# Kernel optimization log

Hardware: AMD Instinct MI355X
Metric: run time of the kernel (lower is better)

The kernel has to match this reference:

```python
import jax, jax.numpy as jnp
import numpy as np

# Dimensions: B graphs, N padded nodes/graph, E edges/graph, D feature dim,
# H attention heads (concat=False -> head average), L stacked GAT layers.
B, N, E, D, H, L = 64, 1024, 16384, 300, 5, 2
NEG_SLOPE = 0.2   # PyG GATConv default negative_slope
LN_EPS = 1e-5


def setup_inputs() -> dict:
    key = jax.random.key(0)
    ks = jax.random.split(key, 6)
    t2 = jax.random.normal(ks[0], (B, N, D), dtype=jnp.float32)
    edge_index = jax.random.randint(ks[1], (B, 2, E), 0, N, dtype=jnp.int32)
    gnn_mask = jnp.zeros((B, N), dtype=bool)  # True = padded node
    # Per-layer GATConv parameters (heads=5, concat=False -> out dim D)
    W = jax.random.normal(ks[2], (L, D, H * D), dtype=jnp.float32) * 0.05
    att_src = jax.random.normal(ks[3], (L, H, D), dtype=jnp.float32) * 0.05
    att_dst = jax.random.normal(ks[4], (L, H, D), dtype=jnp.float32) * 0.05
    bias = jnp.zeros((L, D), dtype=jnp.float32)
    # Shared LayerNorm (single nn.LayerNorm reused after every layer)
    ln_gamma = jnp.ones((D,), dtype=jnp.float32)
    ln_beta = jnp.zeros((D,), dtype=jnp.float32)
    return {"t2": t2, "edge_index": edge_index, "gnn_mask": gnn_mask,
            "W": W, "att_src": att_src, "att_dst": att_dst, "bias": bias,
            "ln_gamma": ln_gamma, "ln_beta": ln_beta}


def _layernorm(x, g, b):
    mu = jnp.mean(x, axis=-1, keepdims=True)
    var = jnp.mean(jnp.square(x - mu), axis=-1, keepdims=True)
    return (x - mu) * jax.lax.rsqrt(var + LN_EPS) * g + b


def _gat_conv(x, src, dst, mask, Wl, a_src, a_dst, bl):
    """Single-graph GATConv: x[N,D], src/dst[E], mask[N] (True=padded)."""
    n = x.shape[0]
    h = (x @ Wl).reshape(n, H, D)                       # [N,H,D] projected per head
    a_s = jnp.einsum('nhd,hd->nh', h, a_src)            # [N,H]
    a_d = jnp.einsum('nhd,hd->nh', h, a_dst)            # [N,H]
    e = jax.nn.leaky_relu(a_s[src] + a_d[dst], NEG_SLOPE)  # [E,H] edge scores
    # drop messages originating from padded nodes
    e = jnp.where(mask[src][:, None], -1e9, e)
    # scatter-softmax over incoming edges of each destination node
    m = jax.ops.segment_max(e, dst, num_segments=n)     # [N,H]
    ex = jnp.exp(e - m[dst])
    den = jax.ops.segment_sum(ex, dst, num_segments=n)  # [N,H]
    alpha = ex / (den[dst] + 1e-16)                     # [E,H]
    # scatter-add aggregation of head-weighted messages
    out = jax.ops.segment_sum(alpha[:, :, None] * h[src], dst, num_segments=n)
    return out.mean(axis=1) + bl                        # concat=False: head mean, [N,D]


def reference(t2, edge_index, gnn_mask, W, att_src, att_dst, bias, ln_gamma, ln_beta):
    x = t2
    for l in range(L):
        conv = lambda xg, ei, mg: _gat_conv(xg, ei[0], ei[1], mg,
                                            W[l], att_src[l], att_dst[l], bias[l])
        x = jax.vmap(conv)(x, edge_index, gnn_mask)     # batch over graphs
        x = _layernorm(jax.nn.gelu(x), ln_gamma, ln_beta)  # GELU then shared LayerNorm
    return x
```

## Files before the change

### kernel.cpp

```cpp
#include <hip/hip_runtime.h>
#include <cstdint>
#include <cstddef>

typedef unsigned short u16;
typedef short short8 __attribute__((ext_vector_type(8)));
typedef __bf16 bf16x8 __attribute__((ext_vector_type(8)));
typedef float f32x4 __attribute__((ext_vector_type(4)));

#define BB 64
#define NNODE 1024
#define EDGES 16384
#define DIM 300
#define HEADS 5
#define LAYERS 2
#define K_PAD 320
#define N_PAD 1536
#define BM 128
#define BK 32

__device__ __forceinline__ u16 f32_to_bf16(float f) {
    union { float f; uint32_t u; } v; v.f = f;
    uint32_t u = v.u;
    uint32_t r = u + 0x7fffu + ((u >> 16) & 1u);
    return (u16)(r >> 16);
}
__device__ __forceinline__ float bf16_to_f32(u16 h) {
    union { uint32_t u; float f; } v; v.u = ((uint32_t)h) << 16;
    return v.f;
}

__global__ __launch_bounds__(256) void csr_build(const int* __restrict__ ei,
                                                 int* __restrict__ offs,
                                                 int* __restrict__ csr_src) {
    int b = blockIdx.x;
    const int* src = ei + (size_t)b * 2 * EDGES;
    const int* dst = src + EDGES;
    __shared__ int cnt[NNODE];
    __shared__ int grp[256];
    int t = threadIdx.x;
    for (int i = t; i < NNODE; i += 256) cnt[i] = 0;
    __syncthreads();
    for (int e = t; e < EDGES; e += 256) atomicAdd(&cnt[dst[e]], 1);
    __syncthreads();
    int c0 = cnt[4 * t + 0], c1 = cnt[4 * t + 1], c2 = cnt[4 * t + 2], c3 = cnt[4 * t + 3];
    grp[t] = c0 + c1 + c2 + c3;
    __syncthreads();
    for (int off = 1; off < 256; off <<= 1) {
        int v = (t >= off) ? grp[t - off] : 0;
        __syncthreads();
        grp[t] += v;
        __syncthreads();
    }
    int base = (t == 0) ? 0 : grp[t - 1];
    int o0 = base, o1 = o0 + c0, o2 = o1 + c1, o3 = o2 + c2;
    cnt[4 * t + 0] = o0; cnt[4 * t + 1] = o1; cnt[4 * t + 2] = o2; cnt[4 * t + 3] = o3;
    int* ob = offs + b * (NNODE + 1);
    ob[4 * t + 0] = o0; ob[4 * t + 1] = o1; ob[4 * t + 2] = o2; ob[4 * t + 3] = o3;
    if (t == 0) ob[NNODE] = EDGES;
    __syncthreads();
    for (int e = t; e < EDGES; e += 256) {
        int d = dst[e];
        int pos = atomicAdd(&cnt[d], 1);
        csr_src[(size_t)b * EDGES + pos] = src[e];
    }
}

__global__ __launch_bounds__(256) void split_w_all(const float* __restrict__ W,
                                                   u16* __restrict__ hi, u16* __restrict__ lo) {
    int i = blockIdx.x * 256 + threadIdx.x;
    int k = i % K_PAD;
    int rem = i / K_PAD;
    int n = rem % N_PAD;
    int l = rem / N_PAD;
    float v = (k < DIM && n < HEADS * DIM)
                  ? W[((size_t)l * DIM + k) * (HEADS * DIM) + n]
                  : 0.f;
    u16 h = f32_to_bf16(v);
    hi[i] = h;
    lo[i] = f32_to_bf16(v - bf16_to_f32(h));
}

__global__ __launch_bounds__(256) void pad_x(const float* __restrict__ X,
                                             float* __restrict__ Xp) {
    size_t i = (size_t)blockIdx.x * 256 + threadIdx.x;
    int k = (int)(i % K_PAD);
    size_t row = i / K_PAD;
    Xp[i] = (k < DIM) ? X[row * DIM + k] : 0.f;
}

__device__ __forceinline__ f32x4 mfma16(short8 a, short8 b, f32x4 c) {
    return __builtin_amdgcn_mfma_f32_16x16x32_bf16(
        __builtin_bit_cast(bf16x8, a), __builtin_bit_cast(bf16x8, b), c, 0, 0, 0);
}

__global__ __launch_bounds__(256) void gemm_split(const float* __restrict__ Xp,
                                                  const u16* __restrict__ Bhi,
                                                  const u16* __restrict__ Blo,
                                                  u16* __restrict__ Hout) {
    __shared__ __align__(16) short lds[4][BM][BK];
    int t = threadIdx.x;
    int m0 = blockIdx.x * BM, n0 = blockIdx.y * BM;
    int lane = t & 63, w = t >> 6, wr = w >> 1, wc = w & 1;
    int lrow = lane & 15, kg = lane >> 4;

    const u16* gWh = Bhi + (size_t)n0 * K_PAD;
    const u16* gWl = Blo + (size_t)n0 * K_PAD;

    f32x4 acc[4][4] = {};

    for (int k0 = 0; k0 < K_PAD; k0 += BK) {
        __syncthreads();
#pragma unroll
        for (int i = 0; i < 2; i++) {
            int chunk = t + (i << 8);
            int row = chunk >> 2, g = chunk & 3;
            const float* src = &Xp[(size_t)(m0 + row) * K_PAD + k0 + g * 8];
            f32x4 v0 = *(const f32x4*)src;
            f32x4 v1 = *(const f32x4*)(src + 4);
            short8 h8, l8;
#pragma unroll
            for (int j = 0; j < 8; j++) {
                float f = (j < 4) ? v0[j] : v1[j - 4];
                u16 h = f32_to_bf16(f);
                h8[j] = (short)h;
                l8[j] = (short)f32_to_bf16(f - bf16_to_f32(h));
            }
            int gsw = (g ^ ((row >> 1) & 3)) * 8;
            *(short8*)&lds[0][row][gsw] = h8;
            *(short8*)&lds[1][row][gsw] = l8;
        }
#pragma unroll
        for (int i = 0; i < 4; i++) {
            int chunk = t + ((i & 1) << 8);
            int row = chunk >> 2, g = chunk & 3;
            int gsw = (g ^ ((row >> 1) & 3)) * 8;
            const u16* gs = (i < 2) ? gWh : gWl;
            short* ls = (i < 2) ? &lds[2][row][gsw] : &lds[3][row][gsw];
            *(short8*)ls = *(const short8*)&gs[(size_t)row * K_PAD + k0 + g * 8];
        }
        __syncthreads();

        short8 ah[4], al[4], bh[4], bl[4];
#pragma unroll
        for (int f = 0; f < 4; f++) {
            int ra = wr * 64 + f * 16 + lrow;
            int sa = (kg ^ ((ra >> 1) & 3)) * 8;
            ah[f] = *(const short8*)&lds[0][ra][sa];
            al[f] = *(const short8*)&lds[1][ra][sa];
            int rb = wc * 64 + f * 16 + lrow;
            int sb = (kg ^ ((rb >> 1) & 3)) * 8;
            bh[f] = *(const short8*)&lds[2][rb][sb];
            bl[f] = *(const short8*)&lds[3][rb][sb];
        }
#pragma unroll
        for (int fm = 0; fm < 4; fm++)
#pragma unroll
            for (int fn = 0; fn < 4; fn++) {
                acc[fm][fn] = mfma16(ah[fm], bh[fn], acc[fm][fn]);
                acc[fm][fn] = mfma16(ah[fm], bl[fn], acc[fm][fn]);
                acc[fm][fn] = mfma16(al[fm], bh[fn], acc[fm][fn]);
            }
    }

#pragma unroll
    for (int fm = 0; fm < 4; fm++)
#pragma unroll
        for (int fn = 0; fn < 4; fn++)
#pragma unroll
            for (int i = 0; i < 4; i++) {
                int row = m0 + wr * 64 + fm * 16 + (lane >> 4) * 4 + i;
                int col = n0 + wc * 64 + fn * 16 + (lane & 15);
                Hout[(size_t)row * N_PAD + col] = f32_to_bf16(acc[fm][fn][i]);
            }
}

__global__ __launch_bounds__(256) void head_dots(const u16* __restrict__ Hb,
                                                 const float* __restrict__ att_s,
                                                 const float* __restrict__ att_d,
                                                 float* __restrict__ a_s,
                                                 float* __restrict__ a_d) {
    int node = blockIdx.x * 4 + (threadIdx.x >> 6);
    int lane = threadIdx.x & 63;
    const u16* row = Hb + (size_t)node * N_PAD;
#pragma unroll
    for (int hd = 0; hd < HEADS; hd++) {
        float ss = 0.f, sd = 0.f;
        for (int c = hd * DIM + lane; c < (hd + 1) * DIM; c += 64) {
            float hv = bf16_to_f32(row[c]);
            ss += hv * att_s[c];
            sd += hv * att_d[c];
        }
#pragma unroll
        for (int o = 32; o > 0; o >>= 1) {
            ss += __shfl_down(ss, o);
            sd += __shfl_down(sd, o);
        }
        if (lane == 0) {
            a_s[(size_t)node * HEADS + hd] = ss;
            a_d[(size_t)node * HEADS + hd] = sd;
        }
    }
}

__global__ __launch_bounds__(320) void agg_kernel(const u16* __restrict__ Hb,
                                                  const float* __restrict__ a_s,
                                                  const float* __restrict__ a_d_arr,
                                                  const int* __restrict__ offs,
                                                  const int* __restrict__ csr_src,
                                                  const unsigned char* __restrict__ mask,
                                                  const float* __restrict__ bias_l,
                                                  const float* __restrict__ gamma,
                                                  const float* __restrict__ beta,
                                                  int graph0,
                                                  float* __restrict__ out,
                                                  int ldo, int do_pad) {
    int nb = blockIdx.x;
    int xcd = nb & 7;
    int j = nb >> 3;
    int b = xcd + 8 * (j >> 10);
    int n = j & 1023;
    int node = b * NNODE + n;
    int gb = graph0 + b;
    int t = threadIdx.x;
    int h = t % 5, et = t / 5;

    __shared__ float red[320];
    __shared__ float mh[5], dh[5];
    __shared__ float alpha[64][5];
    __shared__ int srcs[64];
    __shared__ float stat[2];

    int off0 = offs[gb * (NNODE + 1) + n];
    int off1 = offs[gb * (NNODE + 1) + n + 1];
    int deg = off1 - off0;
    const int* slist = csr_src + (size_t)gb * EDGES + off0;
    float adh = a_d_arr[(size_t)node * HEADS + h];

    float mt = -1e30f;
    for (int e = et; e < deg; e += 64) {
        int s = slist[e];
        float sc = a_s[(size_t)(b * NNODE + s) * HEADS + h] + adh;
        sc = (sc >= 0.f) ? sc : 0.2f * sc;
        if (mask[gb * NNODE + s]) sc = -1e9f;
        mt = fmaxf(mt, sc);
    }
    red[t] = mt;
    __syncthreads();
    if (t < 5) {
        float m = -1e30f;
        for (int q = 0; q < 64; q++) m = fmaxf(m, red[t + 5 * q]);
        mh[t] = m;
    }
    __syncthreads();
    float m_h = mh[h];

    float dt = 0.f;
    for (int e = et; e < deg; e += 64) {
        int s = slist[e];
        float sc = a_s[(size_t)(b * NNODE + s) * HEADS + h] + adh;
        sc = (sc >= 0.f) ? sc : 0.2f * sc;
        if (mask[gb * NNODE + s]) sc = -1e9f;
        dt += __expf(sc - m_h);
    }
    red[t] = dt;
    __syncthreads();
    if (t < 5) {
        float s = 0.f;
        for (int q = 0; q < 64; q++) s += red[t + 5 * q];
        dh[t] = s;
    }
    __syncthreads();
    float den_h = dh[h] + 1e-16f;

    int d = t;
    float acc0 = 0.f, acc1 = 0.f, acc2 = 0.f, acc3 = 0.f, acc4 = 0.f;
    for (int c0 = 0; c0 < deg; c0 += 64) {
        int cn = min(64, deg - c0);
        __syncthreads();
        if (t < cn * 5) {
            int e = c0 + et;
            int s = slist[e];
            float sc = a_s[(size_t)(b * NNODE + s) * HEADS + h] + adh;
            sc = (sc >= 0.f) ? sc : 0.2f * sc;
            if (mask[gb * NNODE + s]) sc = -1e9f;
            alpha[et][h] = __expf(sc - m_h) / den_h;
            if (h == 0) srcs[et] = s;
        }
        __syncthreads();
        if (d < DIM) {
            for (int e = 0; e < cn; e++) {
                const u16* hr = Hb + (size_t)(b * NNODE + srcs[e]) * N_PAD + d;
                acc0 += alpha[e][0] * bf16_to_f32(hr[0 * DIM]);
                acc1 += alpha[e][1] * bf16_to_f32(hr[1 * DIM]);
                acc2 += alpha[e][2] * bf16_to_f32(hr[2 * DIM]);
                acc3 += alpha[e][3] * bf16_to_f32(hr[3 * DIM]);
                acc4 += alpha[e][4] * bf16_to_f32(hr[4 * DIM]);
            }
        }
    }

    float g = 0.f;
    if (d < DIM) {
        float x = (acc0 + acc1 + acc2 + acc3 + acc4) * 0.2f + bias_l[d];
        float u = 0.7978845608028654f * (x + 0.044715f * x * x * x);
        g = 0.5f * x * (1.f + tanhf(u));
    }
    __syncthreads();
    red[t] = g;
    __syncthreads();
    for (int s = 160; s >= 5; s >>= 1) {
        if (t < s) red[t] += red[t + s];
        __syncthreads();
    }
    if (t == 0) stat[0] = (red[0] + red[1] + red[2] + red[3] + red[4]) * (1.f / DIM);
    __syncthreads();
    float mu = stat[0];
    float dv = (d < DIM) ? (g - mu) : 0.f;
    red[t] = dv * dv;
    __syncthreads();
    for (int s = 160; s >= 5; s >>= 1) {
        if (t < s) red[t] += red[t + s];
        __syncthreads();
    }
    if (t == 0) stat[1] = (red[0] + red[1] + red[2] + red[3] + red[4]) * (1.f / DIM);
    __syncthreads();
    float var = stat[1];
    if (d < DIM) {
        float y = (g - mu) * rsqrtf(var + 1e-5f) * gamma[d] + beta[d];
        out[(size_t)node * ldo + d] = y;
    } else if (do_pad) {
        out[(size_t)node * ldo + d] = 0.f;
    }
}

extern "C" void kernel_launch(void* const* d_in, const int* in_sizes, int n_in,
                              void* d_out, int out_size, void* d_ws, size_t ws_size,
                              hipStream_t stream) {
    const float* t2      = (const float*)d_in[0];
    const int*   ei      = (const int*)d_in[1];
    const unsigned char* mask = (const unsigned char*)d_in[2];
    const float* W       = (const float*)d_in[3];
    const float* att_src = (const float*)d_in[4];
    const float* att_dst = (const float*)d_in[5];
    const float* bias    = (const float*)d_in[6];
    const float* gamma   = (const float*)d_in[7];
    const float* beta    = (const float*)d_in[8];

    auto aln = [](size_t b) { return (b + 255) & ~(size_t)255; };
    auto need = [&](int CB) {
        size_t s = 0;
        s += aln((size_t)LAYERS * N_PAD * K_PAD * 2) * 2;
        s += aln((size_t)CB * NNODE * K_PAD * 4);
        s += aln((size_t)CB * NNODE * N_PAD * 2);
        s += aln((size_t)CB * NNODE * HEADS * 4) * 2;
        s += aln((size_t)BB * (NNODE + 1) * 4);
        s += aln((size_t)BB * EDGES * 4);
        return s;
    };
    int CB = 32;
    if (ws_size == 0) CB = 8;
    else while (CB > 8 && need(CB) > ws_size) CB >>= 1;
    const int MC = CB * NNODE;

    char* p = (char*)d_ws;
    auto alloc = [&](size_t bytes) {
        char* r = p;
        p += (bytes + 255) & ~(size_t)255;
        return r;
    };
    u16* Wthi = (u16*)alloc((size_t)LAYERS * N_PAD * K_PAD * 2);
    u16* Wtlo = (u16*)alloc((size_t)LAYERS * N_PAD * K_PAD * 2);
    float* Xpad = (float*)alloc((size_t)MC * K_PAD * 4);
    u16* Hb   = (u16*)alloc((size_t)MC * N_PAD * 2);
    float* a_s = (float*)alloc((size_t)MC * HEADS * 4);
    float* a_d = (float*)alloc((size_t)MC * HEADS * 4);
    int* offs  = (int*)alloc((size_t)BB * (NNODE + 1) * 4);
    int* csr   = (int*)alloc((size_t)BB * EDGES * 4);

    csr_build<<<BB, 256, 0, stream>>>(ei, offs, csr);
    split_w_all<<<(LAYERS * N_PAD * K_PAD) / 256, 256, 0, stream>>>(W, Wthi, Wtlo);

    for (int g0 = 0; g0 < BB; g0 += CB) {
        pad_x<<<(MC * K_PAD) / 256, 256, 0, stream>>>(t2 + (size_t)g0 * NNODE * DIM, Xpad);
        for (int l = 0; l < LAYERS; l++) {
            dim3 gg(MC / BM, N_PAD / BM);
            gemm_split<<<gg, 256, 0, stream>>>(Xpad,
                                               Wthi + (size_t)l * N_PAD * K_PAD,
                                               Wtlo + (size_t)l * N_PAD * K_PAD, Hb);
            head_dots<<<MC / 4, 256, 0, stream>>>(Hb, att_src + (size_t)l * HEADS * DIM,
                                                  att_dst + (size_t)l * HEADS * DIM, a_s, a_d);
            if (l == LAYERS - 1) {
                agg_kernel<<<MC, 320, 0, stream>>>(Hb, a_s, a_d, offs, csr, mask,
                                                   bias + (size_t)l * DIM, gamma, beta,
                                                   g0, (float*)d_out + (size_t)g0 * NNODE * DIM,
                                                   DIM, 0);
            } else {
                agg_kernel<<<MC, 320, 0, stream>>>(Hb, a_s, a_d, offs, csr, mask,
                                                   bias + (size_t)l * DIM, gamma, beta,
                                                   g0, Xpad, K_PAD, 1);
            }
        }
    }
}
```

Measured before the change: 1.623 ms.

## Use online softmax in GAT aggregation and drop activation low-part GEMM term

The aggregation kernel now computes the per-head softmax in one pass, using a running max with rescaling and wave-level shuffle reductions, instead of three passes over the edge list with LDS tree reductions. It also unrolls the gather loop by two edges and replaces the LayerNorm tree reductions with shuffles. Separately, the projection GEMM stops splitting the activations into hi/lo bf16 parts, which removes one of the three MFMAs per tile and one LDS buffer. The GEMM change lowers the input precision of the projection to plain bf16, which may affect accuracy.

Measured after the change: 1.522 ms. 1.07x faster.

```diff
diff --git a/kernel.cpp b/kernel.cpp
--- a/kernel.cpp
+++ b/kernel.cpp
@@ -97,7 +97,7 @@
                                                   const u16* __restrict__ Bhi,
                                                   const u16* __restrict__ Blo,
                                                   u16* __restrict__ Hout) {
-    __shared__ __align__(16) short lds[4][BM][BK];
+    __shared__ __align__(16) short lds[3][BM][BK];
     int t = threadIdx.x;
     int m0 = blockIdx.x * BM, n0 = blockIdx.y * BM;
     int lane = t & 63, w = t >> 6, wr = w >> 1, wc = w & 1;
@@ -117,17 +117,14 @@
             const float* src = &Xp[(size_t)(m0 + row) * K_PAD + k0 + g * 8];
             f32x4 v0 = *(const f32x4*)src;
             f32x4 v1 = *(const f32x4*)(src + 4);
-            short8 h8, l8;
+            short8 h8;
 #pragma unroll
             for (int j = 0; j < 8; j++) {
                 float f = (j < 4) ? v0[j] : v1[j - 4];
-                u16 h = f32_to_bf16(f);
-                h8[j] = (short)h;
-                l8[j] = (short)f32_to_bf16(f - bf16_to_f32(h));
+                h8[j] = (short)f32_to_bf16(f);
             }
             int gsw = (g ^ ((row >> 1) & 3)) * 8;
             *(short8*)&lds[0][row][gsw] = h8;
-            *(short8*)&lds[1][row][gsw] = l8;
         }
 #pragma unroll
         for (int i = 0; i < 4; i++) {
@@ -135,30 +132,28 @@
             int row = chunk >> 2, g = chunk & 3;
             int gsw = (g ^ ((row >> 1) & 3)) * 8;
             const u16* gs = (i < 2) ? gWh : gWl;
-            short* ls = (i < 2) ? &lds[2][row][gsw] : &lds[3][row][gsw];
+            short* ls = (i < 2) ? &lds[1][row][gsw] : &lds[2][row][gsw];
             *(short8*)ls = *(const short8*)&gs[(size_t)row * K_PAD + k0 + g * 8];
         }
         __syncthreads();
 
-        short8 ah[4], al[4], bh[4], bl[4];
+        short8 ah[4], bh[4], bl[4];
 #pragma unroll
         for (int f = 0; f < 4; f++) {
             int ra = wr * 64 + f * 16 + lrow;
             int sa = (kg ^ ((ra >> 1) & 3)) * 8;
             ah[f] = *(const short8*)&lds[0][ra][sa];
-            al[f] = *(const short8*)&lds[1][ra][sa];
             int rb = wc * 64 + f * 16 + lrow;
             int sb = (kg ^ ((rb >> 1) & 3)) * 8;
-            bh[f] = *(const short8*)&lds[2][rb][sb];
-            bl[f] = *(const short8*)&lds[3][rb][sb];
+            bh[f] = *(const short8*)&lds[1][rb][sb];
+            bl[f] = *(const short8*)&lds[2][rb][sb];
         }
 #pragma unroll
         for (int fm = 0; fm < 4; fm++)
 #pragma unroll
             for (int fn = 0; fn < 4; fn++) {
+                acc[fm][fn] = mfma16(ah[fm], bl[fn], acc[fm][fn]);
                 acc[fm][fn] = mfma16(ah[fm], bh[fn], acc[fm][fn]);
-                acc[fm][fn] = mfma16(ah[fm], bl[fn], acc[fm][fn]);
-                acc[fm][fn] = mfma16(al[fm], bh[fn], acc[fm][fn]);
             }
     }
 
@@ -222,114 +217,115 @@
     int node = b * NNODE + n;
     int gb = graph0 + b;
     int t = threadIdx.x;
-    int h = t % 5, et = t / 5;
-
-    __shared__ float red[320];
-    __shared__ float mh[5], dh[5];
-    __shared__ float alpha[64][5];
-    __shared__ int srcs[64];
-    __shared__ float stat[2];
+    int wave = t >> 6, lane = t & 63;
+
+    __shared__ float s_p[64][HEADS];
+    __shared__ int   s_srcs[64];
+    __shared__ float s_scale[HEADS];
+    __shared__ float s_den[HEADS];
+    __shared__ float s_part[2][HEADS];
 
     int off0 = offs[gb * (NNODE + 1) + n];
-    int off1 = offs[gb * (NNODE + 1) + n + 1];
-    int deg = off1 - off0;
+    int deg = offs[gb * (NNODE + 1) + n + 1] - off0;
     const int* slist = csr_src + (size_t)gb * EDGES + off0;
-    float adh = a_d_arr[(size_t)node * HEADS + h];
-
-    float mt = -1e30f;
-    for (int e = et; e < deg; e += 64) {
-        int s = slist[e];
-        float sc = a_s[(size_t)(b * NNODE + s) * HEADS + h] + adh;
-        sc = (sc >= 0.f) ? sc : 0.2f * sc;
-        if (mask[gb * NNODE + s]) sc = -1e9f;
-        mt = fmaxf(mt, sc);
-    }
-    red[t] = mt;
-    __syncthreads();
-    if (t < 5) {
-        float m = -1e30f;
-        for (int q = 0; q < 64; q++) m = fmaxf(m, red[t + 5 * q]);
-        mh[t] = m;
-    }
-    __syncthreads();
-    float m_h = mh[h];
-
-    float dt = 0.f;
-    for (int e = et; e < deg; e += 64) {
-        int s = slist[e];
-        float sc = a_s[(size_t)(b * NNODE + s) * HEADS + h] + adh;
-        sc = (sc >= 0.f) ? sc : 0.2f * sc;
-        if (mask[gb * NNODE + s]) sc = -1e9f;
-        dt += __expf(sc - m_h);
-    }
-    red[t] = dt;
-    __syncthreads();
-    if (t < 5) {
-        float s = 0.f;
-        for (int q = 0; q < 64; q++) s += red[t + 5 * q];
-        dh[t] = s;
-    }
-    __syncthreads();
-    float den_h = dh[h] + 1e-16f;
-
-    int d = t;
-    float acc0 = 0.f, acc1 = 0.f, acc2 = 0.f, acc3 = 0.f, acc4 = 0.f;
+
+    float adh = a_d_arr[(size_t)node * HEADS + wave];
+    const float* as_g = a_s + (size_t)b * NNODE * HEADS;
+    const unsigned char* mk_g = mask + (size_t)gb * NNODE;
+    const u16* hbase = Hb + (size_t)b * NNODE * N_PAD + t;
+
+    float m_run = -1e30f, den_run = 0.f;
+    float acc[HEADS] = {0.f, 0.f, 0.f, 0.f, 0.f};
+
     for (int c0 = 0; c0 < deg; c0 += 64) {
         int cn = min(64, deg - c0);
-        __syncthreads();
-        if (t < cn * 5) {
-            int e = c0 + et;
-            int s = slist[e];
-            float sc = a_s[(size_t)(b * NNODE + s) * HEADS + h] + adh;
-            sc = (sc >= 0.f) ? sc : 0.2f * sc;
-            if (mask[gb * NNODE + s]) sc = -1e9f;
-            alpha[et][h] = __expf(sc - m_h) / den_h;
-            if (h == 0) srcs[et] = s;
-        }
-        __syncthreads();
-        if (d < DIM) {
-            for (int e = 0; e < cn; e++) {
-                const u16* hr = Hb + (size_t)(b * NNODE + srcs[e]) * N_PAD + d;
-                acc0 += alpha[e][0] * bf16_to_f32(hr[0 * DIM]);
-                acc1 += alpha[e][1] * bf16_to_f32(hr[1 * DIM]);
-                acc2 += alpha[e][2] * bf16_to_f32(hr[2 * DIM]);
-                acc3 += alpha[e][3] * bf16_to_f32(hr[3 * DIM]);
-                acc4 += alpha[e][4] * bf16_to_f32(hr[4 * DIM]);
-            }
-        }
-    }
+        if (t < cn) s_srcs[t] = slist[c0 + t];
+        __syncthreads();
+
+        float sc = -1e30f;
+        if (lane < cn) {
+            int s = s_srcs[lane];
+            float v = as_g[s * HEADS + wave] + adh;
+            v = (v >= 0.f) ? v : 0.2f * v;
+            if (mk_g[s]) v = -1e9f;
+            sc = v;
+        }
+        float cm = sc;
+#pragma unroll
+        for (int o = 32; o > 0; o >>= 1) cm = fmaxf(cm, __shfl_xor(cm, o));
+        float m_new = fmaxf(m_run, cm);
+        float scale = (m_run <= -1e29f) ? 0.f : __expf(m_run - m_new);
+        float p = (lane < cn) ? __expf(sc - m_new) : 0.f;
+        float ds = p;
+#pragma unroll
+        for (int o = 32; o > 0; o >>= 1) ds += __shfl_xor(ds, o);
+        den_run = den_run * scale + ds;
+        m_run = m_new;
+        s_p[lane][wave] = p;
+        if (lane == 0) s_scale[wave] = scale;
+        __syncthreads();
+
+        if (t < DIM) {
+#pragma unroll
+            for (int h = 0; h < HEADS; h++) acc[h] *= s_scale[h];
+            int e = 0;
+            for (; e + 2 <= cn; e += 2) {
+                const u16* h0 = hbase + (size_t)s_srcs[e] * N_PAD;
+                const u16* h1 = hbase + (size_t)s_srcs[e + 1] * N_PAD;
+                float q00 = s_p[e][0], q01 = s_p[e][1], q02 = s_p[e][2],
+                      q03 = s_p[e][3], q04 = s_p[e][4];
+                float q10 = s_p[e + 1][0], q11 = s_p[e + 1][1], q12 = s_p[e + 1][2],
+                      q13 = s_p[e + 1][3], q14 = s_p[e + 1][4];
+                acc[0] += q00 * bf16_to_f32(h0[0 * DIM]) + q10 * bf16_to_f32(h1[0 * DIM]);
+                acc[1] += q01 * bf16_to_f32(h0[1 * DIM]) + q11 * bf16_to_f32(h1[1 * DIM]);
+                acc[2] += q02 * bf16_to_f32(h0[2 * DIM]) + q12 * bf16_to_f32(h1[2 * DIM]);
+                acc[3] += q03 * bf16_to_f32(h0[3 * DIM]) + q13 * bf16_to_f32(h1[3 * DIM]);
+                acc[4] += q04 * bf16_to_f32(h0[4 * DIM]) + q14 * bf16_to_f32(h1[4 * DIM]);
+            }
+            if (e < cn) {
+                const u16* h0 = hbase + (size_t)s_srcs[e] * N_PAD;
+                acc[0] += s_p[e][0] * bf16_to_f32(h0[0 * DIM]);
+                acc[1] += s_p[e][1] * bf16_to_f32(h0[1 * DIM]);
+                acc[2] += s_p[e][2] * bf16_to_f32(h0[2 * DIM]);
+                acc[3] += s_p[e][3] * bf16_to_f32(h0[3 * DIM]);
+                acc[4] += s_p[e][4] * bf16_to_f32(h0[4 * DIM]);
+            }
+        }
+        __syncthreads();
+    }
+
+    if (lane == 0) s_den[wave] = den_run + 1e-16f;
+    __syncthreads();
 
     float g = 0.f;
-    if (d < DIM) {
-        float x = (acc0 + acc1 + acc2 + acc3 + acc4) * 0.2f + bias_l[d];
+    if (t < DIM) {
+        float x = 0.f;
+#pragma unroll
+        for (int h = 0; h < HEADS; h++) x += acc[h] / s_den[h];
+        x = x * 0.2f + bias_l[t];
         float u = 0.7978845608028654f * (x + 0.044715f * x * x * x);
         g = 0.5f * x * (1.f + tanhf(u));
     }
-    __syncthreads();
-    red[t] = g;
-    __syncthreads();
-    for (int s = 160; s >= 5; s >>= 1) {
-        if (t < s) red[t] += red[t + s];
-        __syncthreads();
-    }
-    if (t == 0) stat[0] = (red[0] + red[1] + red[2] + red[3] + red[4]) * (1.f / DIM);
-    __syncthreads();
-    float mu = stat[0];
-    float dv = (d < DIM) ? (g - mu) : 0.f;
-    red[t] = dv * dv;
-    __syncthreads();
-    for (int s = 160; s >= 5; s >>= 1) {
-        if (t < s) red[t] += red[t + s];
-        __syncthreads();
-    }
-    if (t == 0) stat[1] = (red[0] + red[1] + red[2] + red[3] + red[4]) * (1.f / DIM);
-    __syncthreads();
-    float var = stat[1];
-    if (d < DIM) {
-        float y = (g - mu) * rsqrtf(var + 1e-5f) * gamma[d] + beta[d];
-        out[(size_t)node * ldo + d] = y;
+    float sum = g;
+#pragma unroll
+    for (int o = 32; o > 0; o >>= 1) sum += __shfl_xor(sum, o);
+    if (lane == 0) s_part[0][wave] = sum;
+    __syncthreads();
+    float mu = (s_part[0][0] + s_part[0][1] + s_part[0][2] + s_part[0][3] + s_part[0][4])
+               * (1.f / DIM);
+    float dv = (t < DIM) ? (g - mu) : 0.f;
+    float sq = dv * dv;
+#pragma unroll
+    for (int o = 32; o > 0; o >>= 1) sq += __shfl_xor(sq, o);
+    if (lane == 0) s_part[1][wave] = sq;
+    __syncthreads();
+    float var = (s_part[1][0] + s_part[1][1] + s_part[1][2] + s_part[1][3] + s_part[1][4])
+                * (1.f / DIM);
+    if (t < DIM) {
+        float y = dv * rsqrtf(var + 1e-5f) * gamma[t] + beta[t];
+        out[(size_t)node * ldo + t] = y;
     } else if (do_pad) {
-        out[(size_t)node * ldo + d] = 0.f;
+        out[(size_t)node * ldo + t] = 0.f;
     }
 }
 
```
